# Performance work log

Hardware: AMD Instinct MI355X
Metric: run time of the kernel (lower is better)

## Reference

```python
import jax, jax.numpy as jnp
import numpy as np

WINDOW_SIZE = 11
CHANNEL = 1
SIGMA = 1.5


def _gaussian_window(window_size=WINDOW_SIZE, channel=CHANNEL, sigma=SIGMA):
    x = np.arange(window_size)
    g = np.exp(-((x - window_size // 2) ** 2) / (2.0 * sigma ** 2))
    g = g / g.sum()
    w2d = np.outer(g, g).astype(np.float32)  # [K,K]
    # depthwise conv kernel: [C_out=channel, C_in/groups=1, K, K]
    return jnp.asarray(np.broadcast_to(w2d, (channel, 1, window_size, window_size)))


def _dwconv(x, window):
    pad = WINDOW_SIZE // 2
    return jax.lax.conv_general_dilated(
        x, window,
        window_strides=(1, 1),
        padding=[(pad, pad), (pad, pad)],
        dimension_numbers=('NCHW', 'OIHW', 'NCHW'),
        feature_group_count=CHANNEL)


def _ssim(img1, img2, window):
    C1 = 0.01 ** 2
    C2 = 0.03 ** 2
    mu1 = _dwconv(img1, window)
    mu2 = _dwconv(img2, window)
    mu1_sq = mu1 * mu1
    mu2_sq = mu2 * mu2
    mu1_mu2 = mu1 * mu2
    sigma1_sq = _dwconv(img1 * img1, window) - mu1_sq
    sigma2_sq = _dwconv(img2 * img2, window) - mu2_sq
    sigma12 = _dwconv(img1 * img2, window) - mu1_mu2
    ssim_map = ((2.0 * mu1_mu2 + C1) * (2.0 * sigma12 + C2)) / (
        (mu1_sq + mu2_sq + C1) * (sigma1_sq + sigma2_sq + C2))
    return ssim_map.mean()


def setup_inputs() -> dict:
    key = jax.random.key(0)
    k1, k2 = jax.random.split(key)
    B, C, H, W = 64, 1, 512, 512
    pred = jax.random.uniform(k1, (B, C, H, W), dtype=jnp.float32)
    target = jax.random.uniform(k2, (B, C, H, W), dtype=jnp.float32)
    return {"pred": pred, "target": target}


def reference(pred, target):
    window = _gaussian_window()
    return 1.0 - _ssim(pred[:, :1], target[:, :1], window)
```

## Files before the change

### kernel.cpp

```cpp
#include <hip/hip_runtime.h>

#define BATCH 64
#define HH 512
#define WW 512
#define TH 32
#define KS 11
#define PADK 5
#define RCH 4
#define NCH 11
#define NPIX (64.0 * 512.0 * 512.0)
#define LROW (WW + 2 * PADK)

__global__ void __launch_bounds__(WW, 4) ssim_main_kernel(
    const float* __restrict__ img1, const float* __restrict__ img2,
    double* __restrict__ accum) {
  constexpr float G[KS] = {
      0.00102838f, 0.00759884f, 0.03600087f, 0.10936069f, 0.21300553f,
      0.26601172f, 0.21300553f, 0.10936069f, 0.03600087f, 0.00759884f,
      0.00102838f};

  const int c  = threadIdx.x;
  const int r0 = blockIdx.x * TH;
  const int b  = blockIdx.y;

  const float* __restrict__ p1 = img1 + (size_t)b * (HH * WW);
  const float* __restrict__ p2 = img2 + (size_t)b * (HH * WW);

  __shared__ float4 s4[2][RCH][LROW];
  if (c < PADK) {
#pragma unroll
    for (int bi = 0; bi < 2; ++bi)
#pragma unroll
      for (int r = 0; r < RCH; ++r) {
        s4[bi][r][c]             = make_float4(0.f, 0.f, 0.f, 0.f);
        s4[bi][r][WW + PADK + c] = make_float4(0.f, 0.f, 0.f, 0.f);
      }
  }

  float rA[KS], rB[KS], rQ[KS], rP[KS];
  float local = 0.f;

  float pa[RCH], pb[RCH];
#pragma unroll
  for (int r = 0; r < RCH; ++r) {
    const int rr = r0 - PADK + r;
    pa[r] = 0.f; pb[r] = 0.f;
    if (rr >= 0 && rr < HH) {
      const int off = rr * WW + c;
      pa[r] = p1[off];
      pb[r] = p2[off];
    }
  }

#pragma unroll
  for (int ii = 0; ii < NCH; ++ii) {
    const int buf = ii & 1;

#pragma unroll
    for (int r = 0; r < RCH; ++r) {
      const float a = pa[r], bb = pb[r];
      s4[buf][r][PADK + c] = make_float4(a, bb, fmaf(a, a, bb * bb), a * bb);
    }
    __syncthreads();

    if (ii + 1 < NCH) {
#pragma unroll
      for (int r = 0; r < RCH; ++r) {
        const int rr = r0 - PADK + (ii + 1) * RCH + r;
        pa[r] = 0.f; pb[r] = 0.f;
        if (rr >= 0 && rr < HH) {
          const int off = rr * WW + c;
          pa[r] = p1[off];
          pb[r] = p2[off];
        }
      }
    }

#pragma unroll
    for (int p = 0; p < RCH; ++p) {
      const int i = ii * RCH + p;

      float h1 = 0.f, h2 = 0.f, hq = 0.f, hp = 0.f;
#pragma unroll
      for (int k = 0; k < KS; ++k) {
        const float4 v = s4[buf][p][c + k];
        const float w  = G[k];
        h1 = fmaf(w, v.x, h1);
        h2 = fmaf(w, v.y, h2);
        hq = fmaf(w, v.z, hq);
        hp = fmaf(w, v.w, hp);
      }

      rA[i % KS] = h1; rB[i % KS] = h2; rQ[i % KS] = hq; rP[i % KS] = hp;

      if (i >= 2 * PADK && i < TH + 2 * PADK) {
        float mu1 = 0.f, mu2 = 0.f, mq = 0.f, mp = 0.f;
#pragma unroll
        for (int t = 0; t < KS; ++t) {
          const int s = (i + 1 + t) % KS;
          const float w = G[t];
          mu1 = fmaf(w, rA[s], mu1);
          mu2 = fmaf(w, rB[s], mu2);
          mq  = fmaf(w, rQ[s], mq);
          mp  = fmaf(w, rP[s], mp);
        }
        const float mu1s = mu1 * mu1;
        const float mu2s = mu2 * mu2;
        const float mu12 = mu1 * mu2;
        const float s12 = mp - mu12;
        const float sqq = mq - mu1s - mu2s;
        const float C1 = 1e-4f, C2 = 9e-4f;
        const float num = fmaf(2.f, mu12, C1) * fmaf(2.f, s12, C2);
        const float den = (mu1s + mu2s + C1) * (sqq + C2);
        local = fmaf(num, __builtin_amdgcn_rcpf(den), local);
      }
    }
  }

#pragma unroll
  for (int off = 32; off > 0; off >>= 1) local += __shfl_down(local, off, 64);

  __shared__ float wsum[WW / 64];
  const int wave = threadIdx.x >> 6;
  const int lane = threadIdx.x & 63;
  if (lane == 0) wsum[wave] = local;
  __syncthreads();
  if (threadIdx.x == 0) {
    float s = 0.f;
#pragma unroll
    for (int w = 0; w < WW / 64; ++w) s += wsum[w];
    atomicAdd(accum, (double)s);
  }
}

__global__ void ssim_final_kernel(const double* __restrict__ accum,
                                  float* __restrict__ out) {
  out[0] = 1.0f - (float)(accum[0] / NPIX);
}

extern "C" void kernel_launch(void* const* d_in, const int* in_sizes, int n_in,
                              void* d_out, int out_size, void* d_ws, size_t ws_size,
                              hipStream_t stream) {
  const float* img1 = (const float*)d_in[0];
  const float* img2 = (const float*)d_in[1];
  double* accum = (double*)d_ws;
  hipMemsetAsync(accum, 0, sizeof(double), stream);

  dim3 grid(HH / TH, BATCH);
  ssim_main_kernel<<<grid, WW, 0, stream>>>(img1, img2, accum);
  ssim_final_kernel<<<1, 1, 0, stream>>>(accum, (float*)d_out);
}
```

Before: 185.2 us.

## Compute two output columns per thread with float2 loads and 11-row ring buffer

Each block now uses 256 threads, and each thread produces two adjacent output columns. Pixels are loaded as float2 and stored into an 11-row shared ring as interleaved (a,b) pairs, and the squared and product terms are computed on the fly instead of being stored. Horizontal taps are read as six float4 loads covering 12 columns and shared between the two outputs, which cuts LDS traffic per output. The cost is doubled register arrays (two sets of 11-deep vertical histories for four quantities), which raises register pressure and may lower occupancy, and the load/compute phasing within each chunk is rearranged.

```diff
diff --git a/kernel.cpp b/kernel.cpp
--- a/kernel.cpp
+++ b/kernel.cpp
@@ -6,129 +6,154 @@
 #define TH 32
 #define KS 11
 #define PADK 5
-#define RCH 4
-#define NCH 11
+#define NIN (TH + 2 * PADK)
+#define NCHK 4
+#define PADL 5
+#define LROW2 (PADL + WW + PADL)
 #define NPIX (64.0 * 512.0 * 512.0)
-#define LROW (WW + 2 * PADK)
 
-__global__ void __launch_bounds__(WW, 4) ssim_main_kernel(
+__global__ void __launch_bounds__(256, 3) ssim_main_kernel(
     const float* __restrict__ img1, const float* __restrict__ img2,
     double* __restrict__ accum) {
   constexpr float G[KS] = {
       0.00102838f, 0.00759884f, 0.03600087f, 0.10936069f, 0.21300553f,
       0.26601172f, 0.21300553f, 0.10936069f, 0.03600087f, 0.00759884f,
       0.00102838f};
+  const float C1 = 1e-4f, C2 = 9e-4f;
 
-  const int c  = threadIdx.x;
+  const int t  = threadIdx.x;
   const int r0 = blockIdx.x * TH;
   const int b  = blockIdx.y;
 
-  const float* __restrict__ p1 = img1 + (size_t)b * (HH * WW);
-  const float* __restrict__ p2 = img2 + (size_t)b * (HH * WW);
+  const float2* __restrict__ pp1 =
+      reinterpret_cast<const float2*>(img1 + (size_t)b * HH * WW);
+  const float2* __restrict__ pp2 =
+      reinterpret_cast<const float2*>(img2 + (size_t)b * HH * WW);
 
-  __shared__ float4 s4[2][RCH][LROW];
-  if (c < PADK) {
+  __shared__ __align__(16) float2 s2[KS][LROW2];
+  __shared__ float wsum[256 / 64];
+
+  if (t < 2 * PADK) {
+    const int slot = (t < PADK) ? t : (WW + PADL + t - PADK);
 #pragma unroll
-    for (int bi = 0; bi < 2; ++bi)
-#pragma unroll
-      for (int r = 0; r < RCH; ++r) {
-        s4[bi][r][c]             = make_float4(0.f, 0.f, 0.f, 0.f);
-        s4[bi][r][WW + PADK + c] = make_float4(0.f, 0.f, 0.f, 0.f);
-      }
+    for (int r = 0; r < KS; ++r) s2[r][slot] = make_float2(0.f, 0.f);
   }
 
-  float rA[KS], rB[KS], rQ[KS], rP[KS];
+  float rA[2][KS], rB[2][KS], rQ[2][KS], rP[2][KS];
+  float2 qa[6], qb[6];
   float local = 0.f;
 
-  float pa[RCH], pb[RCH];
-#pragma unroll
-  for (int r = 0; r < RCH; ++r) {
-    const int rr = r0 - PADK + r;
-    pa[r] = 0.f; pb[r] = 0.f;
-    if (rr >= 0 && rr < HH) {
-      const int off = rr * WW + c;
-      pa[r] = p1[off];
-      pb[r] = p2[off];
-    }
+#define LOADHALF(cn_, p0_, n_)                                           \
+  {                                                                      \
+    const int cb_ = 11 * (cn_) + (p0_);                                  \
+    _Pragma("unroll")                                                    \
+    for (int j = 0; j < (n_); ++j) {                                     \
+      const int rr_ = r0 - PADK + cb_ + j;                               \
+      qa[j] = make_float2(0.f, 0.f);                                     \
+      qb[j] = make_float2(0.f, 0.f);                                     \
+      if (rr_ >= 0 && rr_ < HH && (cb_ + j) < NIN) {                     \
+        qa[j] = pp1[(size_t)rr_ * (WW / 2) + t];                         \
+        qb[j] = pp2[(size_t)rr_ * (WW / 2) + t];                         \
+      }                                                                  \
+    }                                                                    \
   }
 
-#pragma unroll
-  for (int ii = 0; ii < NCH; ++ii) {
-    const int buf = ii & 1;
+#define WRITEHALF(p0_, n_)                                               \
+  {                                                                      \
+    _Pragma("unroll")                                                    \
+    for (int j = 0; j < (n_); ++j) {                                     \
+      s2[(p0_) + j][PADL + 2 * t]     = make_float2(qa[j].x, qb[j].x);   \
+      s2[(p0_) + j][PADL + 2 * t + 1] = make_float2(qa[j].y, qb[j].y);   \
+    }                                                                    \
+  }
 
-#pragma unroll
-    for (int r = 0; r < RCH; ++r) {
-      const float a = pa[r], bb = pb[r];
-      s4[buf][r][PADK + c] = make_float4(a, bb, fmaf(a, a, bb * bb), a * bb);
-    }
+#define ROWS(o_, p0_, n_)                                                \
+  {                                                                      \
+    _Pragma("unroll")                                                    \
+    for (int pj = 0; pj < (n_); ++pj) {                                  \
+      const int p_ = (p0_) + pj;                \
+      const int i_ = 11 * (o_) + p_;                  \
+      if (i_ < NIN) {                                                    \
+        const float4* r4_ = reinterpret_cast<const float4*>(&s2[p_][0]); \
+        float ax[12], bx[12];                                            \
+        _Pragma("unroll")                                                \
+        for (int k = 0; k < 6; ++k) {                                    \
+          const float4 v_ = r4_[t + k];                                  \
+          ax[2 * k]     = v_.x; bx[2 * k]     = v_.y;                    \
+          ax[2 * k + 1] = v_.z; bx[2 * k + 1] = v_.w;                    \
+        }                                                                \
+        float h0a = 0.f, h0b = 0.f, h0q = 0.f, h0p = 0.f;                \
+        float h1a = 0.f, h1b = 0.f, h1q = 0.f, h1p = 0.f;                \
+        _Pragma("unroll")                                                \
+        for (int j = 0; j < 12; ++j) {                                   \
+          const float qv_ = fmaf(ax[j], ax[j], bx[j] * bx[j]);           \
+          const float pv_ = ax[j] * bx[j];                               \
+          if (j < KS) {                                                  \
+            const float w_ = G[j];                                       \
+            h0a = fmaf(w_, ax[j], h0a); h0b = fmaf(w_, bx[j], h0b);      \
+            h0q = fmaf(w_, qv_, h0q);   h0p = fmaf(w_, pv_, h0p);        \
+          }                                                              \
+          if (j >= 1) {                                                  \
+            const float w_ = G[j - 1];                                   \
+            h1a = fmaf(w_, ax[j], h1a); h1b = fmaf(w_, bx[j], h1b);      \
+            h1q = fmaf(w_, qv_, h1q);   h1p = fmaf(w_, pv_, h1p);        \
+          }                                                              \
+        }                                                                \
+        rA[0][p_] = h0a; rB[0][p_] = h0b; rQ[0][p_] = h0q; rP[0][p_] = h0p; \
+        rA[1][p_] = h1a; rB[1][p_] = h1b; rQ[1][p_] = h1q; rP[1][p_] = h1p; \
+        if (i_ >= 2 * PADK) {                                            \
+           \
+          _Pragma("unroll")                                              \
+          for (int u = 0; u < 2; ++u) {                                  \
+            float m1 = 0.f, m2 = 0.f, mq = 0.f, mp = 0.f;                \
+            _Pragma("unroll")                                            \
+            for (int tt = 0; tt < KS; ++tt) {                            \
+              const int sl_ = (p_ + 1 + tt) % KS;                        \
+              const float w_ = G[tt];                                    \
+              m1 = fmaf(w_, rA[u][sl_], m1);                             \
+              m2 = fmaf(w_, rB[u][sl_], m2);                             \
+              mq = fmaf(w_, rQ[u][sl_], mq);                             \
+              mp = fmaf(w_, rP[u][sl_], mp);                             \
+            }                                                            \
+            const float m1s = m1 * m1, m2s = m2 * m2, m12 = m1 * m2;     \
+            const float s12 = mp - m12;                                  \
+            const float sqq = mq - m1s - m2s;                            \
+            const float num = fmaf(2.f, m12, C1) * fmaf(2.f, s12, C2);   \
+            const float den = (m1s + m2s + C1) * (sqq + C2);             \
+            local = fmaf(num, __builtin_amdgcn_rcpf(den), local);        \
+          }                                                              \
+        }                                                                \
+      }                                                                  \
+    }                                                                    \
+  }
+
+  LOADHALF(0, 0, 6);
+  WRITEHALF(0, 6);
+  LOADHALF(0, 6, 5);
+  WRITEHALF(6, 5);
+  __syncthreads();
+
+#pragma unroll 1
+  for (int o = 0; o < NCHK; ++o) {
+    const int nx = o + 1;
+    if (nx < NCHK) LOADHALF(nx, 0, 6);
+    ROWS(o, 0, 6);
     __syncthreads();
-
-    if (ii + 1 < NCH) {
-#pragma unroll
-      for (int r = 0; r < RCH; ++r) {
-        const int rr = r0 - PADK + (ii + 1) * RCH + r;
-        pa[r] = 0.f; pb[r] = 0.f;
-        if (rr >= 0 && rr < HH) {
-          const int off = rr * WW + c;
-          pa[r] = p1[off];
-          pb[r] = p2[off];
-        }
-      }
-    }
-
-#pragma unroll
-    for (int p = 0; p < RCH; ++p) {
-      const int i = ii * RCH + p;
-
-      float h1 = 0.f, h2 = 0.f, hq = 0.f, hp = 0.f;
-#pragma unroll
-      for (int k = 0; k < KS; ++k) {
-        const float4 v = s4[buf][p][c + k];
-        const float w  = G[k];
-        h1 = fmaf(w, v.x, h1);
-        h2 = fmaf(w, v.y, h2);
-        hq = fmaf(w, v.z, hq);
-        hp = fmaf(w, v.w, hp);
-      }
-
-      rA[i % KS] = h1; rB[i % KS] = h2; rQ[i % KS] = hq; rP[i % KS] = hp;
-
-      if (i >= 2 * PADK && i < TH + 2 * PADK) {
-        float mu1 = 0.f, mu2 = 0.f, mq = 0.f, mp = 0.f;
-#pragma unroll
-        for (int t = 0; t < KS; ++t) {
-          const int s = (i + 1 + t) % KS;
-          const float w = G[t];
-          mu1 = fmaf(w, rA[s], mu1);
-          mu2 = fmaf(w, rB[s], mu2);
-          mq  = fmaf(w, rQ[s], mq);
-          mp  = fmaf(w, rP[s], mp);
-        }
-        const float mu1s = mu1 * mu1;
-        const float mu2s = mu2 * mu2;
-        const float mu12 = mu1 * mu2;
-        const float s12 = mp - mu12;
-        const float sqq = mq - mu1s - mu2s;
-        const float C1 = 1e-4f, C2 = 9e-4f;
-        const float num = fmaf(2.f, mu12, C1) * fmaf(2.f, s12, C2);
-        const float den = (mu1s + mu2s + C1) * (sqq + C2);
-        local = fmaf(num, __builtin_amdgcn_rcpf(den), local);
-      }
-    }
+    if (nx < NCHK) WRITEHALF(0, 6);
+    if (nx < NCHK) LOADHALF(nx, 6, 5);
+    ROWS(o, 6, 5);
+    __syncthreads();
+    if (nx < NCHK) WRITEHALF(6, 5);
   }
 
 #pragma unroll
   for (int off = 32; off > 0; off >>= 1) local += __shfl_down(local, off, 64);
-
-  __shared__ float wsum[WW / 64];
-  const int wave = threadIdx.x >> 6;
-  const int lane = threadIdx.x & 63;
+  const int wave = t >> 6;
+  const int lane = t & 63;
   if (lane == 0) wsum[wave] = local;
   __syncthreads();
-  if (threadIdx.x == 0) {
-    float s = 0.f;
-#pragma unroll
-    for (int w = 0; w < WW / 64; ++w) s += wsum[w];
+  if (t == 0) {
+    float s = wsum[0] + wsum[1] + wsum[2] + wsum[3];
     atomicAdd(accum, (double)s);
   }
 }
@@ -147,6 +172,6 @@
   hipMemsetAsync(accum, 0, sizeof(double), stream);
 
   dim3 grid(HH / TH, BATCH);
-  ssim_main_kernel<<<grid, WW, 0, stream>>>(img1, img2, accum);
+  ssim_main_kernel<<<grid, 256, 0, stream>>>(img1, img2, accum);
   ssim_final_kernel<<<1, 1, 0, stream>>>(accum, (float*)d_out);
 }
```

Result: slower. 243.4 us (+31.4%).
